# Performance work log

Hardware: AMD Instinct MI355X
Metric: run time of the kernel (lower is better)

## Reference

```python
import jax, jax.numpy as jnp
import numpy as np

NUM_HEADS = 2
ROPE_BASE = 10000.0


def _rope_tables(seq_len, head_dim, dtype):
    # inv_freq over even indices of head_dim
    inv_freq = 1.0 / (ROPE_BASE ** (jnp.arange(0, head_dim, 2, dtype=jnp.float32) / head_dim))
    t = jnp.arange(seq_len, dtype=jnp.float32)
    freqs = t[:, None] * inv_freq[None, :]            # (s, head_dim/2)
    emb = jnp.concatenate([freqs, freqs], axis=-1)    # (s, head_dim)
    return jnp.cos(emb).astype(dtype), jnp.sin(emb).astype(dtype)


def _apply_rotation(x_bsd, cos, sin):
    # x_bsd: (b, s, h*d); chunk in half along last dim (h=2 -> halves == head_dim)
    x1, x2 = jnp.split(x_bsd, 2, axis=-1)
    return jnp.concatenate([x1 * cos - x2 * sin, x2 * cos + x1 * sin], axis=-1)


def setup_inputs() -> dict:
    key = jax.random.key(0)
    k1, k2, k3, k4 = jax.random.split(key, 4)
    b, s, dim = 4, 2048, 2048
    x = jax.random.normal(k1, (b, s, dim), dtype=jnp.float32)
    wqkv = jax.random.normal(k2, (dim, 3 * dim), dtype=jnp.float32) * (dim ** -0.5)
    wout = jax.random.normal(k3, (dim, dim), dtype=jnp.float32) * (dim ** -0.5)
    bout = jax.random.normal(k4, (dim,), dtype=jnp.float32) * 0.01
    return {"x": x, "wqkv": wqkv, "wout": wout, "bout": bout}


def reference(x, wqkv, wout, bout):
    b, s, dim = x.shape
    h = NUM_HEADS
    d = dim // h
    scale = d ** -0.5

    qkv = x @ wqkv                                    # (b, s, 3*dim)
    qkv = qkv.reshape(b, s, 3, h, d).transpose(2, 0, 3, 1, 4)  # (3, b, h, s, d)
    q, k, v = qkv[0], qkv[1], qkv[2]                  # (b, h, s, d)

    # RoPE applied on (b, s, h*d) layout, exactly as source
    cos, sin = _rope_tables(s, d, x.dtype)            # (s, d) each
    q_flat = q.transpose(0, 2, 1, 3).reshape(b, s, h * d)
    k_flat = k.transpose(0, 2, 1, 3).reshape(b, s, h * d)
    q = _apply_rotation(q_flat, cos, sin).reshape(b, s, h, d).transpose(0, 2, 1, 3)
    k = _apply_rotation(k_flat, cos, sin).reshape(b, s, h, d).transpose(0, 2, 1, 3)

    scores = jnp.einsum('bhid,bhjd->bhij', q, k) * scale
    attn = jax.nn.softmax(scores, axis=-1)
    out = jnp.einsum('bhij,bhjd->bhid', attn, v)      # (b, h, s, d)
    out = out.transpose(0, 2, 1, 3).reshape(b, s, dim)
    return out @ wout + bout
```

## Files before the change

### kernel.cpp

```cpp
#include <hip/hip_runtime.h>
#include <hip/hip_fp16.h>

typedef __attribute__((ext_vector_type(4))) float f32x4;
typedef __attribute__((ext_vector_type(8))) _Float16 f16x8;
typedef __attribute__((ext_vector_type(4))) _Float16 f16x4;

__device__ __forceinline__ void gload_lds16(const void* gp, void* lp) {
    __builtin_amdgcn_global_load_lds(
        (const __attribute__((address_space(1))) void*)gp,
        (__attribute__((address_space(3))) void*)lp, 16, 0, 0);
}

__device__ __forceinline__ void barrier_fenced() {
    asm volatile("s_barrier" ::: "memory");
}

__global__ void rope_tables_k(float* __restrict__ cosT, float* __restrict__ sinT) {
    int idx = blockIdx.x * 256 + threadIdx.x;
    int s = idx >> 9, j = idx & 511;
    float invf = exp2f(-13.287712379549449f * (float)j * (1.0f / 512.0f));
    float ang = (float)s * invf;
    float sn, cs;
    sincosf(ang, &sn, &cs);
    cosT[idx] = cs;
    sinT[idx] = sn;
}

__global__ void f32_to_f16_vec(const float* __restrict__ in, _Float16* __restrict__ out) {
    long i = ((long)blockIdx.x * 256 + threadIdx.x) * 4;
    f32x4 v = *(const f32x4*)(in + i);
    f16x4 h;
#pragma unroll
    for (int e = 0; e < 4; ++e) h[e] = (_Float16)v[e];
    *(f16x4*)(out + i) = h;
}

__global__ void transpose_f32_to_f16(const float* __restrict__ in, _Float16* __restrict__ out,
                                     int R, int C) {
    __shared__ _Float16 tile[32][36];
    const int c0 = blockIdx.x * 32, r0 = blockIdx.y * 32;
    const int t = threadIdx.x;
    const int r = t >> 3, c4 = (t & 7) * 4;
    f32x4 v = *(const f32x4*)(in + (long)(r0 + r) * C + c0 + c4);
    f16x4 h;
#pragma unroll
    for (int e = 0; e < 4; ++e) h[e] = (_Float16)v[e];
    *(f16x4*)&tile[r][c4] = h;
    __syncthreads();
    const int oc = t >> 3, o4 = (t & 7) * 4;
    f16x4 o;
#pragma unroll
    for (int e = 0; e < 4; ++e) o[e] = tile[o4 + e][oc];
    *(f16x4*)(out + (long)(c0 + oc) * R + r0 + o4) = o;
}

__global__ void rope_inplace(_Float16* __restrict__ qkv, const float* __restrict__ cosT,
                             const float* __restrict__ sinT) {
    const int row = blockIdx.x;
    const int s = row & 2047;
    const int j0 = threadIdx.x * 4;
    _Float16* base = qkv + (long)row * 6144;
    f16x4 q0 = *(const f16x4*)(base + j0);
    f16x4 q1 = *(const f16x4*)(base + 1024 + j0);
    f16x4 k0 = *(const f16x4*)(base + 2048 + j0);
    f16x4 k1 = *(const f16x4*)(base + 3072 + j0);
    const int jj = j0 & 511;
    f32x4 cs = *(const f32x4*)(cosT + (long)s * 512 + jj);
    f32x4 sn = *(const f32x4*)(sinT + (long)s * 512 + jj);
    f16x4 oq0, oq1, ok0, ok1;
#pragma unroll
    for (int e = 0; e < 4; ++e) {
        float a = (float)q0[e], b = (float)q1[e];
        oq0[e] = (_Float16)(a * cs[e] - b * sn[e]);
        oq1[e] = (_Float16)(b * cs[e] + a * sn[e]);
        float c = (float)k0[e], d = (float)k1[e];
        ok0[e] = (_Float16)(c * cs[e] - d * sn[e]);
        ok1[e] = (_Float16)(d * cs[e] + c * sn[e]);
    }
    *(f16x4*)(base + j0) = oq0;
    *(f16x4*)(base + 1024 + j0) = oq1;
    *(f16x4*)(base + 2048 + j0) = ok0;
    *(f16x4*)(base + 3072 + j0) = ok1;
}

__global__ void v_transpose(const _Float16* __restrict__ qkv, _Float16* __restrict__ vT) {
    __shared__ _Float16 tile[32][36];
    const int z = blockIdx.z, b = z >> 1, h = z & 1;
    const int s0 = blockIdx.x * 32, d0 = blockIdx.y * 32;
    const int t = threadIdx.x;
    const int r = t >> 3, c4 = (t & 7) * 4;
    const _Float16* src = qkv + (long)(b * 2048 + s0 + r) * 6144 + 4096 + h * 1024 + d0 + c4;
    *(f16x4*)&tile[r][c4] = *(const f16x4*)src;
    __syncthreads();
    const int dr = t >> 3, sc = (t & 7) * 4;
    f16x4 o;
#pragma unroll
    for (int e = 0; e < 4; ++e) o[e] = tile[sc + e][dr];
    *(f16x4*)(vT + ((long)z * 1024 + d0 + dr) * 2048 + s0 + sc) = o;
}

__global__ __launch_bounds__(256) void softmax_rows_f32(float* __restrict__ S, float scale) {
    const int wid = threadIdx.x >> 6, lane = threadIdx.x & 63;
    const long row = (long)blockIdx.x * 4 + wid;
    float* rp = S + row * 2048;
    f32x4 v[8];
    float mx = -1e30f;
#pragma unroll
    for (int i = 0; i < 8; ++i) {
        v[i] = *(const f32x4*)(rp + (i * 64 + lane) * 4);
#pragma unroll
        for (int e = 0; e < 4; ++e) mx = fmaxf(mx, v[i][e]);
    }
#pragma unroll
    for (int o = 32; o > 0; o >>= 1) mx = fmaxf(mx, __shfl_xor(mx, o, 64));
    float sum = 0.f;
#pragma unroll
    for (int i = 0; i < 8; ++i)
#pragma unroll
        for (int e = 0; e < 4; ++e) {
            float p = __expf(scale * (v[i][e] - mx));
            v[i][e] = p; sum += p;
        }
#pragma unroll
    for (int o = 32; o > 0; o >>= 1) sum += __shfl_xor(sum, o, 64);
    float inv = 1.0f / sum;
    _Float16* wp = (_Float16*)S + row * 4096;
#pragma unroll
    for (int i = 0; i < 8; ++i) {
        f16x4 h;
#pragma unroll
        for (int e = 0; e < 4; ++e) h[e] = (_Float16)(v[i][e] * inv);
        *(f16x4*)(wp + (i * 64 + lane) * 4) = h;
    }
}

__global__ __launch_bounds__(256) void rowsum_f16(const _Float16* __restrict__ S,
                                                  float* __restrict__ l) {
    const int wid = threadIdx.x >> 6, lane = threadIdx.x & 63;
    const long row = (long)blockIdx.x * 4 + wid;
    const _Float16* rp = S + row * 2048;
    float sum = 0.f;
#pragma unroll
    for (int i = 0; i < 4; ++i) {
        f16x8 v = *(const f16x8*)(rp + i * 512 + lane * 8);
#pragma unroll
        for (int e = 0; e < 8; ++e) sum += (float)v[e];
    }
#pragma unroll
    for (int o = 32; o > 0; o >>= 1) sum += __shfl_xor(sum, o, 64);
    if (lane == 0) l[row] = sum;
}

template <int OMODE, bool BIAS, bool SWZ>
__global__ __launch_bounds__(512, 2)
void gemm256(const _Float16* __restrict__ A, const _Float16* __restrict__ B,
             void* __restrict__ Cv, const float* __restrict__ aux, float scale,
             int K, int lda, int ldb, int ldc, int zmod,
             long a1, long a2, long b1, long b2, long c1, long c2) {
    __shared__ char lds[131072];
    int sbx, sby, sbz;
    if (SWZ) {
        const int gx = gridDim.x, gy = gridDim.y;
        const int nwg = gx * gy * gridDim.z;
        const int orig = (blockIdx.z * gy + blockIdx.y) * gx + blockIdx.x;
        const int q8 = nwg >> 3, r8 = nwg & 7;
        const int xcd = orig & 7, sub = orig >> 3;
        const int wgid = (xcd < r8 ? xcd * (q8 + 1) : r8 * (q8 + 1) + (xcd - r8) * q8) + sub;
        sbx = wgid % gx;
        const int tmp = wgid / gx;
        sby = tmp % gy; sbz = tmp / gy;
    } else {
        sbx = blockIdx.x; sby = blockIdx.y; sbz = blockIdx.z;
    }

    const int z = sbz, zq = z / zmod, zr = z - zq * zmod;
    A += zq * a1 + zr * a2;
    B += zq * b1 + zr * b2;
    const long coff = zq * c1 + zr * c2;
    const int tm = sby * 256, tn = sbx * 256;
    const int t = threadIdx.x;
    const int lane = t & 63, wid = t >> 6;
    const int wr = wid >> 2, wc = wid & 3;
    const int fr = lane & 15, kg = lane >> 4;

    const int strow = wid * 16 + (lane >> 3);
    const int stcol = ((lane & 7) ^ (lane >> 3)) * 8;
    const _Float16* gA = A + (long)(tm + strow) * lda + stcol;
    const _Float16* gB = B + (long)(tn + strow) * ldb + stcol;
    char* const ldsw = lds + wid * 2048;

    const int sw0 = 16 * ((0 * 4 + kg) ^ (fr & 7));
    const int sw1 = 16 * ((1 * 4 + kg) ^ (fr & 7));

    const int NT = K >> 6;
    f32x4 acc[8][4] = {};

    auto stageA = [&](int tt, int h) {
        const _Float16* s = gA + (long)(h * 128) * lda + tt * 64;
        char* d = ldsw + (tt & 1) * 65536 + h * 16384;
        gload_lds16(s, d);
        gload_lds16(s + (long)8 * lda, d + 1024);
    };
    auto stageB = [&](int tt, int h) {
        const _Float16* s = gB + (long)(h * 128) * ldb + tt * 64;
        char* d = ldsw + (tt & 1) * 65536 + 32768 + h * 16384;
        gload_lds16(s, d);
        gload_lds16(s + (long)8 * ldb, d + 1024);
    };

    stageB(0, 0); stageB(0, 1); stageA(0, 0); stageA(0, 1);
    stageB(1, 0); stageB(1, 1);
    asm volatile("s_waitcnt vmcnt(4)" ::: "memory");
    barrier_fenced();

    f16x8 bf0[2][2], bf1[2][2];
    const int arow = (wr * 128 + fr) * 128;
    const int brow = 32768 + (wc * 64 + fr) * 128;

    for (int g = 0; g < NT; ++g) {
        const char* buf = lds + (g & 1) * 65536;
        f16x8 af0[4][2];
#pragma unroll
        for (int m = 0; m < 4; ++m) {
            af0[m][0] = *(const f16x8*)(buf + arow + m * 2048 + sw0);
            af0[m][1] = *(const f16x8*)(buf + arow + m * 2048 + sw1);
        }
#pragma unroll
        for (int n = 0; n < 2; ++n) {
            bf0[n][0] = *(const f16x8*)(buf + brow + n * 2048 + sw0);
            bf0[n][1] = *(const f16x8*)(buf + brow + n * 2048 + sw1);
            bf1[n][0] = *(const f16x8*)(buf + brow + 4096 + n * 2048 + sw0);
            bf1[n][1] = *(const f16x8*)(buf + brow + 4096 + n * 2048 + sw1);
        }
        if (g + 1 < NT) { stageA(g + 1, 0); stageA(g + 1, 1); }
        __builtin_amdgcn_s_setprio(1);
#pragma unroll
        for (int m = 0; m < 4; ++m)
#pragma unroll
            for (int n = 0; n < 2; ++n)
#pragma unroll
                for (int k = 0; k < 2; ++k) {
                    acc[m][n]     = __builtin_amdgcn_mfma_f32_16x16x32_f16(af0[m][k], bf0[n][k], acc[m][n], 0, 0, 0);
                    acc[m][n + 2] = __builtin_amdgcn_mfma_f32_16x16x32_f16(af0[m][k], bf1[n][k], acc[m][n + 2], 0, 0, 0);
                }
        __builtin_amdgcn_s_setprio(0);
        barrier_fenced();
        f16x8 af1[4][2];
#pragma unroll
        for (int m = 0; m < 4; ++m) {
            af1[m][0] = *(const f16x8*)(buf + arow + 8192 + m * 2048 + sw0);
            af1[m][1] = *(const f16x8*)(buf + arow + 8192 + m * 2048 + sw1);
        }
        if (g + 2 < NT) { stageB(g + 2, 0); stageB(g + 2, 1); }
        __builtin_amdgcn_s_setprio(1);
#pragma unroll
        for (int m = 0; m < 4; ++m)
#pragma unroll
            for (int n = 0; n < 2; ++n)
#pragma unroll
                for (int k = 0; k < 2; ++k) {
                    acc[m + 4][n + 2] = __builtin_amdgcn_mfma_f32_16x16x32_f16(af1[m][k], bf1[n][k], acc[m + 4][n + 2], 0, 0, 0);
                    acc[m + 4][n]     = __builtin_amdgcn_mfma_f32_16x16x32_f16(af1[m][k], bf0[n][k], acc[m + 4][n], 0, 0, 0);
                }
        __builtin_amdgcn_s_setprio(0);
        if (g + 2 < NT)      asm volatile("s_waitcnt vmcnt(4)" ::: "memory");
        else if (g + 1 < NT) asm volatile("s_waitcnt vmcnt(0)" ::: "memory");
        barrier_fenced();
    }

    const int rb = tm + wr * 128 + (lane >> 4) * 4;
    const int cb = tn + wc * 64 + fr;
    const float* auxz = (OMODE == 3) ? (aux + (long)z * 2048) : aux;
#pragma unroll
    for (int m = 0; m < 8; ++m) {
#pragma unroll
        for (int r = 0; r < 4; ++r) {
            const int row = rb + m * 16 + r;
            float inv = 1.0f;
            if (OMODE == 3) inv = __builtin_amdgcn_rcpf(auxz[row]);
#pragma unroll
            for (int n = 0; n < 4; ++n) {
                float v = acc[m][n][r];
                const int col = cb + n * 16;
                if (BIAS) v += aux[col];
                if (OMODE == 0) {
                    ((float*)Cv)[coff + (long)row * ldc + col] = v;
                } else {
                    if (OMODE == 2) v = __expf(v * scale);
                    if (OMODE == 3) v *= inv;
                    ((_Float16*)Cv)[coff + (long)row * ldc + col] = (_Float16)v;
                }
            }
        }
    }
}

extern "C" void kernel_launch(void* const* d_in, const int* in_sizes, int n_in,
                              void* d_out, int out_size, void* d_ws, size_t ws_size,
                              hipStream_t stream) {
    const float* x    = (const float*)d_in[0];
    const float* wqkv = (const float*)d_in[1];
    const float* wout = (const float*)d_in[2];
    const float* bout = (const float*)d_in[3];
    char* ws = (char*)d_ws;

    _Float16* qkv_h = (_Float16*)(ws);
    _Float16* x_h   = (_Float16*)(ws + 100663296);
    _Float16* wqkvT = (_Float16*)(ws + 134217728);
    _Float16* vT    = (_Float16*)(ws + 100663296);
    float*    cosT  = (float*)(ws + 100663296);
    float*    sinT  = (float*)(ws + 104857600);
    _Float16* woutT = (_Float16*)(ws);
    const bool batched = ws_size >= 234946560ULL;

    f32_to_f16_vec<<<dim3(16384), dim3(256), 0, stream>>>(x, x_h);
    transpose_f32_to_f16<<<dim3(192, 64), dim3(256), 0, stream>>>(wqkv, wqkvT, 2048, 6144);
    gemm256<1, false, false><<<dim3(24, 32, 1), dim3(512), 0, stream>>>(
        x_h, wqkvT, (void*)qkv_h, nullptr, 0.f, 2048, 2048, 2048, 6144,
        1, 0L, 0L, 0L, 0L, 0L, 0L);
    rope_tables_k<<<dim3(4096), dim3(256), 0, stream>>>(cosT, sinT);
    rope_inplace<<<dim3(8192), dim3(256), 0, stream>>>(qkv_h, cosT, sinT);
    v_transpose<<<dim3(64, 32, 8), dim3(256), 0, stream>>>(qkv_h, vT);

    if (batched) {
        _Float16* S16  = (_Float16*)(ws + 134217728);
        _Float16* aout = (_Float16*)(ws + 201326592);
        float*    lsum = (float*)(ws + 234881024);
        gemm256<2, false, true><<<dim3(8, 8, 8), dim3(512), 0, stream>>>(
            qkv_h, qkv_h + 2048, (void*)S16, nullptr, 0.03125f, 1024, 6144, 6144, 2048,
            2, 12582912L, 1024L, 12582912L, 1024L, 8388608L, 4194304L);
        rowsum_f16<<<dim3(4096), dim3(256), 0, stream>>>(S16, lsum);
        gemm256<3, false, true><<<dim3(4, 8, 8), dim3(512), 0, stream>>>(
            S16, vT, (void*)aout, lsum, 0.f, 2048, 2048, 2048, 2048,
            2, 8388608L, 4194304L, 4194304L, 2097152L, 4194304L, 1024L);
        transpose_f32_to_f16<<<dim3(64, 64), dim3(256), 0, stream>>>(wout, woutT, 2048, 2048);
        gemm256<0, true, false><<<dim3(8, 32, 1), dim3(512), 0, stream>>>(
            aout, woutT, d_out, bout, 0.f, 2048, 2048, 2048, 2048,
            1, 0L, 0L, 0L, 0L, 0L, 0L);
    } else {
        float*    S32  = (float*)(ws + 134217728);
        _Float16* aout = (_Float16*)(ws + 150994944);
        for (int z = 0; z < 8; ++z) {
            const _Float16* Az = qkv_h + (long)(z >> 1) * 12582912 + (z & 1) * 1024;
            gemm256<0, false, false><<<dim3(8, 8, 1), dim3(512), 0, stream>>>(
                Az, Az + 2048, (void*)S32, nullptr, 0.f, 1024, 6144, 6144, 2048,
                1, 0L, 0L, 0L, 0L, 0L, 0L);
            softmax_rows_f32<<<dim3(512), dim3(256), 0, stream>>>(S32, 0.03125f);
            gemm256<1, false, false><<<dim3(4, 8, 1), dim3(512), 0, stream>>>(
                (const _Float16*)S32, vT + (long)z * 2097152,
                (void*)(aout + (long)(z >> 1) * 4194304 + (z & 1) * 1024), nullptr, 0.f,
                2048, 4096, 2048, 2048, 1, 0L, 0L, 0L, 0L, 0L, 0L);
        }
        transpose_f32_to_f16<<<dim3(64, 64), dim3(256), 0, stream>>>(wout, woutT, 2048, 2048);
        gemm256<0, true, false><<<dim3(8, 32, 1), dim3(512), 0, stream>>>(
            aout, woutT, d_out, bout, 0.f, 2048, 2048, 2048, 2048,
            1, 0L, 0L, 0L, 0L, 0L, 0L);
    }
}
```

Measured before the change: 484.5 us.

## Triple-buffer B tiles in LDS to drop mid-iteration barrier in GEMM

The GEMM main loop's B operand moves from a double buffer to a three-slot ring in LDS, growing shared memory from 128KB to 160KB. Each slot now lies two iterations back from the one being written, so the barrier between the two MFMA half-phases of each k-step is removed. Without it, waves no longer wait for every other wave to finish reading B before the next B prefetch is issued. The cost is more LDS per block, which uses all 160KB per CU and leaves no room for any other block.

```diff
diff --git a/kernel.cpp b/kernel.cpp
--- a/kernel.cpp
+++ b/kernel.cpp
@@ -157,7 +157,7 @@
              void* __restrict__ Cv, const float* __restrict__ aux, float scale,
              int K, int lda, int ldb, int ldc, int zmod,
              long a1, long a2, long b1, long b2, long c1, long c2) {
-    __shared__ char lds[131072];
+    __shared__ char lds[163840];
     int sbx, sby, sbz;
     if (SWZ) {
         const int gx = gridDim.x, gy = gridDim.y;
@@ -187,50 +187,52 @@
     const int stcol = ((lane & 7) ^ (lane >> 3)) * 8;
     const _Float16* gA = A + (long)(tm + strow) * lda + stcol;
     const _Float16* gB = B + (long)(tn + strow) * ldb + stcol;
-    char* const ldsw = lds + wid * 2048;
+    const int ldsw = wid * 2048;
 
     const int sw0 = 16 * ((0 * 4 + kg) ^ (fr & 7));
     const int sw1 = 16 * ((1 * 4 + kg) ^ (fr & 7));
+    const int arowo = (wr * 128 + fr) * 128;
+    const int browo = (wc * 64 + fr) * 128;
 
     const int NT = K >> 6;
     f32x4 acc[8][4] = {};
 
     auto stageA = [&](int tt, int h) {
         const _Float16* s = gA + (long)(h * 128) * lda + tt * 64;
-        char* d = ldsw + (tt & 1) * 65536 + h * 16384;
+        char* d = lds + (tt & 1) * 32768 + h * 16384 + ldsw;
         gload_lds16(s, d);
         gload_lds16(s + (long)8 * lda, d + 1024);
     };
     auto stageB = [&](int tt, int h) {
         const _Float16* s = gB + (long)(h * 128) * ldb + tt * 64;
-        char* d = ldsw + (tt & 1) * 65536 + 32768 + h * 16384;
+        char* d = lds + 65536 + (tt % 3) * 32768 + h * 16384 + ldsw;
         gload_lds16(s, d);
         gload_lds16(s + (long)8 * ldb, d + 1024);
     };
 
-    stageB(0, 0); stageB(0, 1); stageA(0, 0); stageA(0, 1);
+    stageB(0, 0); stageB(0, 1);
+    stageA(0, 0); stageA(0, 1);
     stageB(1, 0); stageB(1, 1);
     asm volatile("s_waitcnt vmcnt(4)" ::: "memory");
     barrier_fenced();
 
     f16x8 bf0[2][2], bf1[2][2];
-    const int arow = (wr * 128 + fr) * 128;
-    const int brow = 32768 + (wc * 64 + fr) * 128;
 
     for (int g = 0; g < NT; ++g) {
-        const char* buf = lds + (g & 1) * 65536;
+        const char* abuf = lds + (g & 1) * 32768;
+        const char* bbuf = lds + 65536 + (g % 3) * 32768;
         f16x8 af0[4][2];
 #pragma unroll
         for (int m = 0; m < 4; ++m) {
-            af0[m][0] = *(const f16x8*)(buf + arow + m * 2048 + sw0);
-            af0[m][1] = *(const f16x8*)(buf + arow + m * 2048 + sw1);
+            af0[m][0] = *(const f16x8*)(abuf + arowo + m * 2048 + sw0);
+            af0[m][1] = *(const f16x8*)(abuf + arowo + m * 2048 + sw1);
         }
 #pragma unroll
         for (int n = 0; n < 2; ++n) {
-            bf0[n][0] = *(const f16x8*)(buf + brow + n * 2048 + sw0);
-            bf0[n][1] = *(const f16x8*)(buf + brow + n * 2048 + sw1);
-            bf1[n][0] = *(const f16x8*)(buf + brow + 4096 + n * 2048 + sw0);
-            bf1[n][1] = *(const f16x8*)(buf + brow + 4096 + n * 2048 + sw1);
+            bf0[n][0] = *(const f16x8*)(bbuf + browo + n * 2048 + sw0);
+            bf0[n][1] = *(const f16x8*)(bbuf + browo + n * 2048 + sw1);
+            bf1[n][0] = *(const f16x8*)(bbuf + browo + 4096 + n * 2048 + sw0);
+            bf1[n][1] = *(const f16x8*)(bbuf + browo + 4096 + n * 2048 + sw1);
         }
         if (g + 1 < NT) { stageA(g + 1, 0); stageA(g + 1, 1); }
         __builtin_amdgcn_s_setprio(1);
@@ -244,12 +246,11 @@
                     acc[m][n + 2] = __builtin_amdgcn_mfma_f32_16x16x32_f16(af0[m][k], bf1[n][k], acc[m][n + 2], 0, 0, 0);
                 }
         __builtin_amdgcn_s_setprio(0);
-        barrier_fenced();
         f16x8 af1[4][2];
 #pragma unroll
         for (int m = 0; m < 4; ++m) {
-            af1[m][0] = *(const f16x8*)(buf + arow + 8192 + m * 2048 + sw0);
-            af1[m][1] = *(const f16x8*)(buf + arow + 8192 + m * 2048 + sw1);
+            af1[m][0] = *(const f16x8*)(abuf + arowo + 8192 + m * 2048 + sw0);
+            af1[m][1] = *(const f16x8*)(abuf + arowo + 8192 + m * 2048 + sw1);
         }
         if (g + 2 < NT) { stageB(g + 2, 0); stageB(g + 2, 1); }
         __builtin_amdgcn_s_setprio(1);
```

Measured after the change: 485.4 us. Within noise of the previous version (+0.2%).
